# Kernel optimization log

Measured on AMD Instinct MI355X. Metric: run time of the kernel, lower is better.

The kernel has to match this reference:

```python
import jax, jax.numpy as jnp
import numpy as np

N_NODES = 20000
N_EDGES = 160000
N_GRAPHS = 64
HIDDEN = 128
CTX = 2048
HEADS = 4
NUM_LAYERS = 3
NUM_BINS = 240
MAX_DIST = 30.0
GAMMA = 0.5
BN_EPS = 1e-5
OUT_DIM = 1024


def setup_inputs() -> dict:
    key = jax.random.key(0)
    ks = jax.random.split(key, 32)
    inp = {}
    inp["atom_types"] = jax.random.randint(ks[0], (N_NODES,), 0, 118)
    inp["pos"] = jax.random.normal(ks[1], (N_NODES, 3), dtype=jnp.float32) * 5.0
    inp["edge_index"] = jax.random.randint(ks[2], (2, N_EDGES), 0, N_NODES)
    inp["edge_attr"] = jax.random.uniform(ks[3], (N_EDGES, 5), dtype=jnp.float32)
    inp["batch"] = jnp.sort(jax.random.randint(ks[4], (N_NODES,), 0, N_GRAPHS))
    inp["context_vector"] = jax.random.normal(ks[5], (N_GRAPHS, CTX), dtype=jnp.float32)
    # initial node embedding Linear(118 -> 128)
    inp["emb_W"] = jax.random.normal(ks[6], (118, HIDDEN), dtype=jnp.float32) * 0.05
    inp["emb_b"] = jnp.zeros((HIDDEN,), jnp.float32)
    # RBF positional MLP: Linear(720->128) + BN + ReLU + Linear(128->2048)
    inp["rbf_lin1_W"] = jax.random.normal(ks[7], (3 * NUM_BINS, 128), dtype=jnp.float32) * 0.03
    inp["rbf_lin1_b"] = jnp.zeros((128,), jnp.float32)
    inp["rbf_bn_g"] = jnp.ones((128,), jnp.float32)
    inp["rbf_bn_b"] = jnp.zeros((128,), jnp.float32)
    inp["rbf_bn_m"] = jax.random.normal(ks[8], (128,), dtype=jnp.float32) * 0.1
    inp["rbf_bn_v"] = jax.random.uniform(ks[9], (128,), dtype=jnp.float32, minval=0.5, maxval=1.5)
    inp["rbf_lin2_W"] = jax.random.normal(ks[10], (128, CTX), dtype=jnp.float32) * 0.05
    inp["rbf_lin2_b"] = jnp.zeros((CTX,), jnp.float32)
    # per-layer GAT params (stacked over layers)
    in_dim = HIDDEN + CTX  # 2176
    inp["gat_W"] = jax.random.normal(ks[11], (NUM_LAYERS, in_dim, HEADS * HIDDEN), dtype=jnp.float32) * 0.02
    inp["att_src"] = jax.random.normal(ks[12], (NUM_LAYERS, HEADS, HIDDEN), dtype=jnp.float32) * 0.1
    inp["att_dst"] = jax.random.normal(ks[13], (NUM_LAYERS, HEADS, HIDDEN), dtype=jnp.float32) * 0.1
    inp["gat_bias"] = jnp.zeros((NUM_LAYERS, HIDDEN), jnp.float32)
    inp["bn_g"] = jnp.ones((NUM_LAYERS, HIDDEN), jnp.float32)
    inp["bn_b"] = jnp.zeros((NUM_LAYERS, HIDDEN), jnp.float32)
    inp["bn_m"] = jax.random.normal(ks[14], (NUM_LAYERS, HIDDEN), dtype=jnp.float32) * 0.1
    inp["bn_v"] = jax.random.uniform(ks[15], (NUM_LAYERS, HIDDEN), dtype=jnp.float32, minval=0.5, maxval=1.5)
    # final Linear(128 -> 1024)
    inp["out_W"] = jax.random.normal(ks[16], (HIDDEN, OUT_DIM), dtype=jnp.float32) * 0.05
    inp["out_b"] = jnp.zeros((OUT_DIM,), jnp.float32)
    return inp


def _bn_eval(x, g, b, m, v):
    return (x - m) * jax.lax.rsqrt(v + BN_EPS) * g + b


def _forward(atom_types, pos, edge_index, edge_attr, batch, context_vector,
             emb_W, emb_b, rbf_lin1_W, rbf_lin1_b, rbf_bn_g, rbf_bn_b, rbf_bn_m,
             rbf_bn_v, rbf_lin2_W, rbf_lin2_b, gat_W, att_src, att_dst, gat_bias,
             bn_g, bn_b, bn_m, bn_v, out_W, out_b):
    N = atom_types.shape[0]
    # initial node embedding (one-hot @ W == row gather, but keep faithful math)
    x = jax.nn.one_hot(atom_types, 118, dtype=jnp.float32) @ emb_W + emb_b  # [N,128]
    # RBF positional encoding: [N,3,num_bins] -> [N,720]
    mu = jnp.linspace(-MAX_DIST, MAX_DIST, NUM_BINS, dtype=jnp.float32)
    rbf = jnp.exp(-GAMMA * (pos[..., None] - mu) ** 2).reshape(N, 3 * NUM_BINS)
    h = jax.nn.relu(_bn_eval(rbf @ rbf_lin1_W + rbf_lin1_b, rbf_bn_g, rbf_bn_b, rbf_bn_m, rbf_bn_v))
    pos_emb = h @ rbf_lin2_W + rbf_lin2_b  # [N,2048]
    context = context_vector[batch] + pos_emb  # pos_info == 'add'
    # GAT adds self-loops by default; edge_attr is ignored (edge_dim=None)
    loops = jnp.arange(N)
    src = jnp.concatenate([edge_index[0], loops])  # message source j
    dst = jnp.concatenate([edge_index[1], loops])  # message target i
    for l in range(NUM_LAYERS):
        xc = jnp.concatenate([x, context], axis=1)                  # [N,2176]
        xs = (xc @ gat_W[l]).reshape(N, HEADS, HIDDEN)              # [N,H,C]
        a_src = jnp.einsum('nhc,hc->nh', xs, att_src[l])            # [N,H]
        a_dst = jnp.einsum('nhc,hc->nh', xs, att_dst[l])
        alpha = jax.nn.leaky_relu(a_src[src] + a_dst[dst], 0.2)     # [E+N,H]
        amax = jax.ops.segment_max(alpha, dst, num_segments=N)
        alpha = jnp.exp(alpha - amax[dst])
        denom = jax.ops.segment_sum(alpha, dst, num_segments=N)
        alpha = alpha / jnp.maximum(denom[dst], 1e-16)
        msg = xs[src] * alpha[..., None]                             # [E+N,H,C]
        agg = jax.ops.segment_sum(msg, dst, num_segments=N)          # [N,H,C]
        x_conv = agg.mean(axis=1) + gat_bias[l]                      # concat=False -> head mean
        x_conv = _bn_eval(x_conv, bn_g[l], bn_b[l], bn_m[l], bn_v[l])
        x_conv = jax.nn.gelu(x_conv, approximate=False)
        x = x + x_conv                                               # residual; dropout inactive (eval)
    out = x @ out_W + out_b                                          # [N,1024]
    return jax.ops.segment_sum(out, batch, num_segments=N_GRAPHS)    # global_add_pool -> [B,1024]


def reference(atom_types, pos, edge_index, edge_attr, batch, context_vector,
              emb_W, emb_b, rbf_lin1_W, rbf_lin1_b, rbf_bn_g, rbf_bn_b, rbf_bn_m,
              rbf_bn_v, rbf_lin2_W, rbf_lin2_b, gat_W, att_src, att_dst, gat_bias,
              bn_g, bn_b, bn_m, bn_v, out_W, out_b):
    return _forward(atom_types, pos, edge_index, edge_attr, batch, context_vector,
                    emb_W, emb_b, rbf_lin1_W, rbf_lin1_b, rbf_bn_g, rbf_bn_b,
                    rbf_bn_m, rbf_bn_v, rbf_lin2_W, rbf_lin2_b, gat_W, att_src,
                    att_dst, gat_bias, bn_g, bn_b, bn_m, bn_v, out_W, out_b)
```

## Files before the change

### kernel.cpp

```cpp
#include <hip/hip_runtime.h>
#include <hip/hip_bf16.h>
#include <cstdint>

constexpr int HIDDEN = 128, CTXD = 2048, HEADS = 4, NLAYERS = 3;
constexpr int KRBF = 720, KPAD = 736;
constexpr int KXH = 256;

typedef __bf16 bf16x8 __attribute__((ext_vector_type(8)));
typedef float f32x4 __attribute__((ext_vector_type(4)));

static __device__ __forceinline__ unsigned short f2bf(float f) {
    union { float f; unsigned u; } v; v.f = f;
    unsigned r = v.u + 0x7fffu + ((v.u >> 16) & 1u);
    return (unsigned short)(r >> 16);
}
static __device__ __forceinline__ float bf2f(unsigned short s) {
    union { unsigned u; float f; } v; v.u = ((unsigned)s) << 16; return v.f;
}

__global__ __launch_bounds__(256) void k_tr(const float* __restrict__ src,
                                            unsigned short* __restrict__ dst,
                                            int R, int C) {
    __shared__ unsigned short t[32][34];
    int b = blockIdx.z;
    int c0 = blockIdx.x * 32, r0 = blockIdx.y * 32;
    const float* s = src + (size_t)b * R * C;
    unsigned short* d = dst + (size_t)b * R * C;
    for (int rr = threadIdx.y; rr < 32; rr += 8) {
        int r = r0 + rr, c = c0 + threadIdx.x;
        unsigned short val = 0;
        if (r < R && c < C) val = f2bf(s[(size_t)r * C + c]);
        t[rr][threadIdx.x] = val;
    }
    __syncthreads();
    for (int rr = threadIdx.y; rr < 32; rr += 8) {
        int c = c0 + rr, r = r0 + threadIdx.x;
        if (c < C && r < R) d[(size_t)c * R + r] = t[threadIdx.x][rr];
    }
}

__global__ __launch_bounds__(256) void k_w2bf(const float* __restrict__ W2,
                                              unsigned short* __restrict__ W2bf) {
    int i = blockIdx.x * 256 + threadIdx.x;
    if (i < 128 * CTXD) W2bf[i] = f2bf(W2[i]);
}
__global__ __launch_bounds__(256) void k_cpre(const float* __restrict__ ctx,
                                              const float* __restrict__ b2,
                                              unsigned short* __restrict__ cpre, int NG) {
    int i = blockIdx.x * 256 + threadIdx.x;
    if (i < NG * CTXD) cpre[i] = f2bf(ctx[i] + b2[i % CTXD]);
}
__global__ __launch_bounds__(256) void k_bccopy(const unsigned short* __restrict__ gatWt,
                                                unsigned short* __restrict__ Bc) {
    int i = blockIdx.x * 256 + threadIdx.x;
    if (i >= NLAYERS * 512 * 128) return;
    int lo = i >> 7, k = i & 127;
    Bc[(size_t)lo * KXH + k] = gatWt[(size_t)lo * 2176 + k];
}

__global__ __launch_bounds__(256) void k_trW1(const float* __restrict__ W1,
                                              unsigned short* __restrict__ W1t) {
    int i = blockIdx.x * 256 + threadIdx.x;
    if (i >= 128 * KPAD) return;
    int c = i / KPAD, k = i % KPAD;
    unsigned short v = 0;
    if (k < KRBF) v = f2bf(W1[(size_t)k * 128 + c]);
    W1t[i] = v;
}

__global__ __launch_bounds__(256) void k_embed(const int* __restrict__ at,
                                               const float* __restrict__ W,
                                               const float* __restrict__ b,
                                               float* __restrict__ x,
                                               unsigned short* __restrict__ xh, int N) {
    int i = blockIdx.x * 256 + threadIdx.x;
    if (i >= N * HIDDEN) return;
    int n = i >> 7, c = i & 127;
    float v = W[(size_t)at[n] * HIDDEN + c] + b[c];
    x[i] = v;
    xh[(size_t)n * KXH + c] = f2bf(v);
}

__global__ __launch_bounds__(256) void k_rbf_mfma(const float* __restrict__ pos,
                                                  const unsigned short* __restrict__ W1t,
                                                  const float* __restrict__ b1,
                                                  const float* __restrict__ g,
                                                  const float* __restrict__ bb,
                                                  const float* __restrict__ bm,
                                                  const float* __restrict__ bv,
                                                  unsigned short* __restrict__ xh, int N) {
    constexpr int LDT = 40;
    __shared__ unsigned short As[128 * LDT];
    __shared__ unsigned short Bs[128 * LDT];
    __shared__ float ps[128 * 3];
    const int tid = threadIdx.x;
    const int lane = tid & 63, wid = tid >> 6;
    const int nb = blockIdx.x * 128;
    for (int i = tid; i < 384; i += 256) {
        int n = nb + i / 3;
        ps[i] = (n < N) ? pos[(size_t)n * 3 + (i % 3)] : 1.0e9f;
    }
    __syncthreads();
    const int sr = tid >> 1, sk = (tid & 1) * 16;
    const int wr = (wid >> 1) * 64, wc = (wid & 1) * 64;
    const int fr = lane & 15, kg = lane >> 4;
    f32x4 acc[4][4];
#pragma unroll
    for (int i = 0; i < 4; i++)
#pragma unroll
        for (int j = 0; j < 4; j++)
#pragma unroll
            for (int r = 0; r < 4; r++) acc[i][j][r] = 0.f;
    const float p0 = ps[sr * 3], p1 = ps[sr * 3 + 1], p2 = ps[sr * 3 + 2];
    const unsigned short* bp = W1t + (size_t)sr * KPAD + sk;
    uint4 bv0 = *(const uint4*)bp, bv1 = *(const uint4*)(bp + 8);
    constexpr int NST = KPAD / 32;
    for (int ks = 0; ks < NST; ++ks) {
        unsigned short av[16];
#pragma unroll
        for (int j = 0; j < 16; j++) {
            int kglob = ks * 32 + sk + j;
            float v = 0.f;
            if (kglob < KRBF) {
                int d = kglob / 240, bin = kglob % 240;
                float mu = -30.f + (60.f / 239.f) * (float)bin;
                float p = (d == 0) ? p0 : ((d == 1) ? p1 : p2);
                float df = p - mu;
                v = __expf(-0.5f * df * df);
            }
            av[j] = f2bf(v);
        }
        __syncthreads();
        *(uint4*)&As[sr * LDT + sk] = *(const uint4*)&av[0];
        *(uint4*)&As[sr * LDT + sk + 8] = *(const uint4*)&av[8];
        *(uint4*)&Bs[sr * LDT + sk] = bv0;
        *(uint4*)&Bs[sr * LDT + sk + 8] = bv1;
        __syncthreads();
        if (ks + 1 < NST) {
            const unsigned short* bp2 = W1t + (size_t)sr * KPAD + (ks + 1) * 32 + sk;
            bv0 = *(const uint4*)bp2;
            bv1 = *(const uint4*)(bp2 + 8);
        }
        bf16x8 afr[4], bfr[4];
#pragma unroll
        for (int i = 0; i < 4; i++) {
            afr[i] = *reinterpret_cast<const bf16x8*>(&As[(wr + i * 16 + fr) * LDT + kg * 8]);
            bfr[i] = *reinterpret_cast<const bf16x8*>(&Bs[(wc + i * 16 + fr) * LDT + kg * 8]);
        }
#pragma unroll
        for (int i = 0; i < 4; i++)
#pragma unroll
            for (int j = 0; j < 4; j++)
                acc[i][j] = __builtin_amdgcn_mfma_f32_16x16x32_bf16(afr[i], bfr[j], acc[i][j], 0, 0, 0);
    }
    const int rg = lane >> 4;
#pragma unroll
    for (int i = 0; i < 4; i++) {
#pragma unroll
        for (int j = 0; j < 4; j++) {
            int col = wc + j * 16 + fr;
            float sc = g[col] * rsqrtf(bv[col] + 1e-5f);
            float sh = bb[col] - bm[col] * sc;
            float bc = b1[col];
#pragma unroll
            for (int r = 0; r < 4; r++) {
                int row = nb + wr + i * 16 + rg * 4 + r;
                if (row < N) {
                    float y = (acc[i][j][r] + bc) * sc + sh;
                    y = fmaxf(y, 0.f);
                    xh[(size_t)row * KXH + 128 + col] = f2bf(y);
                }
            }
        }
    }
}

template <int MODE, int DOATT>
__device__ __forceinline__ void gemm_core(unsigned short* As, unsigned short* Bs,
                                          const unsigned short* __restrict__ A, int lda, int M,
                                          const unsigned short* __restrict__ Bt, int ldb, int K,
                                          void* __restrict__ Cout, int ldc,
                                          const int* __restrict__ batch,
                                          const float* __restrict__ cw,
                                          int m0, int n0,
                                          const float* __restrict__ att_s,
                                          const float* __restrict__ att_d,
                                          float* __restrict__ a_src,
                                          float* __restrict__ a_dst) {
    constexpr int LDT = 40;
    const int tid = threadIdx.x;
    const int lane = tid & 63, wid = tid >> 6;
    const int wr = (wid >> 1) * 64, wc = (wid & 1) * 64;
    const int sr = tid >> 1, sk = (tid & 1) * 16;
    f32x4 acc[4][4];
#pragma unroll
    for (int i = 0; i < 4; i++)
#pragma unroll
        for (int j = 0; j < 4; j++)
#pragma unroll
            for (int r = 0; r < 4; r++) acc[i][j][r] = 0.f;
    const int nst = K / 32;
    const int arow = min(m0 + sr, M - 1);
    const unsigned short* ap = A + (size_t)arow * lda + sk;
    const unsigned short* bp = Bt + (size_t)(n0 + sr) * ldb + sk;
    uint4 av0 = *(const uint4*)ap, av1 = *(const uint4*)(ap + 8);
    uint4 bv0 = *(const uint4*)bp, bv1 = *(const uint4*)(bp + 8);
    const int fr = lane & 15, kg = lane >> 4;
    for (int ks = 0; ks < nst; ++ks) {
        __syncthreads();
        *(uint4*)&As[sr * LDT + sk] = av0;
        *(uint4*)&As[sr * LDT + sk + 8] = av1;
        *(uint4*)&Bs[sr * LDT + sk] = bv0;
        *(uint4*)&Bs[sr * LDT + sk + 8] = bv1;
        __syncthreads();
        if (ks + 1 < nst) {
            const unsigned short* ap2 = A + (size_t)arow * lda + (ks + 1) * 32 + sk;
            const unsigned short* bp2 = Bt + (size_t)(n0 + sr) * ldb + (ks + 1) * 32 + sk;
            av0 = *(const uint4*)ap2; av1 = *(const uint4*)(ap2 + 8);
            bv0 = *(const uint4*)bp2; bv1 = *(const uint4*)(bp2 + 8);
        }
        bf16x8 afr[4], bfr[4];
#pragma unroll
        for (int i = 0; i < 4; i++) {
            afr[i] = *reinterpret_cast<const bf16x8*>(&As[(wr + i * 16 + fr) * LDT + kg * 8]);
            bfr[i] = *reinterpret_cast<const bf16x8*>(&Bs[(wc + i * 16 + fr) * LDT + kg * 8]);
        }
#pragma unroll
        for (int i = 0; i < 4; i++)
#pragma unroll
            for (int j = 0; j < 4; j++)
                acc[i][j] = __builtin_amdgcn_mfma_f32_16x16x32_bf16(afr[i], bfr[j], acc[i][j], 0, 0, 0);
    }
    const int rg = lane >> 4;
    float pssum[4][4], pdsum[4][4];
#pragma unroll
    for (int i = 0; i < 4; i++)
#pragma unroll
        for (int r = 0; r < 4; r++) { pssum[i][r] = 0.f; pdsum[i][r] = 0.f; }
#pragma unroll
    for (int i = 0; i < 4; i++) {
#pragma unroll
        for (int j = 0; j < 4; j++) {
            int col = n0 + wc + j * 16 + fr;
            float asw = 0.f, adw = 0.f;
            if (DOATT) { asw = att_s[col]; adw = att_d[col]; }
#pragma unroll
            for (int r = 0; r < 4; r++) {
                int row = m0 + wr + i * 16 + rg * 4 + r;
                if (row < M) {
                    float vv = acc[i][j][r];
                    if (MODE == 2) {
                        ((float*)Cout)[(size_t)row * ldc + col] = vv;
                    } else if (MODE == 3) {
                        vv += cw[(size_t)batch[row] * 512 + col];
                        ((unsigned short*)Cout)[(size_t)row * ldc + col] = f2bf(vv);
                        if (DOATT) { pssum[i][r] += vv * asw; pdsum[i][r] += vv * adw; }
                    } else {
                        ((unsigned short*)Cout)[(size_t)row * ldc + col] = f2bf(vv);
                    }
                }
            }
        }
    }
    if (DOATT) {
        __syncthreads();
        float* lat = (float*)As;
#pragma unroll
        for (int i = 0; i < 4; i++) {
#pragma unroll
            for (int r = 0; r < 4; r++) {
                float s = pssum[i][r], d = pdsum[i][r];
#pragma unroll
                for (int dd = 1; dd < 16; dd <<= 1) {
                    s += __shfl_xor(s, dd);
                    d += __shfl_xor(d, dd);
                }
                if (fr == 0) {
                    int k = i * 16 + rg * 4 + r;
                    lat[(wid * 64 + k) * 2] = s;
                    lat[(wid * 64 + k) * 2 + 1] = d;
                }
            }
        }
        __syncthreads();
        if ((wid & 1) == 0) {
            int k = lane;
            int row = m0 + (wid >> 1) * 64 + k;
            if (row < M) {
                float s = lat[(wid * 64 + k) * 2] + lat[((wid + 1) * 64 + k) * 2];
                float d = lat[(wid * 64 + k) * 2 + 1] + lat[((wid + 1) * 64 + k) * 2 + 1];
                int head = n0 >> 7;
                a_src[(size_t)row * 4 + head] = s;
                a_dst[(size_t)row * 4 + head] = d;
            }
        }
    }
}

__global__ __launch_bounds__(256) void k_gemm3(const unsigned short* __restrict__ A, int M,
                                               const unsigned short* __restrict__ Bt,
                                               unsigned short* __restrict__ C,
                                               const int* __restrict__ batch,
                                               const float* __restrict__ cw,
                                               const float* __restrict__ att_s,
                                               const float* __restrict__ att_d,
                                               float* __restrict__ a_src,
                                               float* __restrict__ a_dst) {
    constexpr int LDT = 40;
    __shared__ unsigned short As[128 * LDT];
    __shared__ unsigned short Bs[128 * LDT];
    gemm_core<3, 1>(As, Bs, A, KXH, M, Bt, KXH, KXH, C, 512, batch, cw,
                    blockIdx.x * 128, blockIdx.y * 128, att_s, att_d, a_src, a_dst);
}

__global__ __launch_bounds__(256) void k_prep(const unsigned short* __restrict__ gatWt,
                                              const unsigned short* __restrict__ W2bf,
                                              const unsigned short* __restrict__ cpre,
                                              unsigned short* __restrict__ Bc,
                                              float* __restrict__ cW, int NG) {
    constexpr int LDT = 40;
    __shared__ unsigned short As[128 * LDT];
    __shared__ unsigned short Bs[128 * LDT];
    int z = blockIdx.z;
    if (z < 3) {
        if (blockIdx.y != 0) return;
        gemm_core<0, 0>(As, Bs, gatWt + (size_t)z * 512 * 2176 + 128, 2176, 512,
                        W2bf, CTXD, CTXD, Bc + (size_t)z * 512 * KXH + 128, KXH,
                        nullptr, nullptr, blockIdx.x * 128, 0,
                        nullptr, nullptr, nullptr, nullptr);
    } else {
        if (blockIdx.x != 0) return;
        int zz = z - 3;
        gemm_core<2, 0>(As, Bs, cpre, CTXD, NG, gatWt + (size_t)zz * 512 * 2176 + 128, 2176, CTXD,
                        cW + (size_t)zz * NG * 512, 512, nullptr, nullptr, 0, blockIdx.y * 128,
                        nullptr, nullptr, nullptr, nullptr);
    }
}

__global__ void k_cnt_init(int* cnt, int N) {
    int i = blockIdx.x * 256 + threadIdx.x;
    if (i < N) cnt[i] = 1;
}
__global__ void k_cnt(const int* __restrict__ ei, int E, int* cnt) {
    int i = blockIdx.x * 256 + threadIdx.x;
    if (i < E) atomicAdd(&cnt[ei[E + i]], 1);
}
__global__ __launch_bounds__(1024) void k_scan(const int* __restrict__ cnt, int* __restrict__ rowptr,
                                               int* __restrict__ cursor, int n) {
    __shared__ int wsum[16];
    __shared__ int carry;
    int tid = threadIdx.x, lane = tid & 63, wid = tid >> 6;
    if (tid == 0) carry = 0;
    __syncthreads();
    for (int basei = 0; basei < n; basei += 1024) {
        int i = basei + tid;
        int v = (i < n) ? cnt[i] : 0;
        int s = v;
#pragma unroll
        for (int d = 1; d < 64; d <<= 1) {
            int t = __shfl_up(s, (unsigned)d);
            if (lane >= d) s += t;
        }
        if (lane == 63) wsum[wid] = s;
        __syncthreads();
        if (wid == 0 && lane < 16) {
            int ws = wsum[lane]; int t = ws;
#pragma unroll
            for (int d = 1; d < 16; d <<= 1) {
                int u = __shfl_up(t, (unsigned)d);
                if (lane >= d) t += u;
            }
            wsum[lane] = t - ws;
        }
        __syncthreads();
        int excl = carry + wsum[wid] + (s - v);
        if (i < n) { rowptr[i] = excl; cursor[i] = excl; }
        __syncthreads();
        if (tid == 1023) carry += wsum[15] + s;
        __syncthreads();
    }
    if (tid == 0) rowptr[n] = carry;
}
__global__ void k_fill(const int* __restrict__ ei, int E, int N, int* cursor, int* csrc) {
    int i = blockIdx.x * 256 + threadIdx.x;
    if (i >= E + N) return;
    int s, d;
    if (i < E) { s = ei[i]; d = ei[E + i]; }
    else { s = i - E; d = s; }
    int slot = atomicAdd(&cursor[d], 1);
    csrc[slot] = s;
}

__global__ __launch_bounds__(256) void k_agg(const int* __restrict__ rowptr,
                                             const int* __restrict__ csrc,
                                             const float* __restrict__ asrc,
                                             const float* __restrict__ adstv,
                                             const unsigned short* __restrict__ xs,
                                             const float* __restrict__ gbias,
                                             const float* __restrict__ bg,
                                             const float* __restrict__ bb,
                                             const float* __restrict__ bm,
                                             const float* __restrict__ bv,
                                             float* __restrict__ x,
                                             unsigned short* __restrict__ xh, int N) {
    __shared__ float wsh[4][64][4];
    __shared__ int ssh[4][64];
    int tid = threadIdx.x, lane = tid & 63, wid = tid >> 6;
    int n = blockIdx.x * 4 + wid;
    if (n >= N) return;
    int beg = rowptr[n], end = rowptr[n + 1];
    float4 ad = *(const float4*)(adstv + (size_t)n * 4);
    int nch = (end - beg + 63) >> 6;
    float m0 = -1e30f, m1 = -1e30f, m2 = -1e30f, m3 = -1e30f;
    float s0 = 0.f, s1 = 0.f, s2 = 0.f, s3 = 0.f;
    float a0 = -1e30f, a1 = -1e30f, a2 = -1e30f, a3 = -1e30f;
    int sv = 0;
    for (int base = beg; base < end; base += 64) {
        int idx = base + lane;
        float b0 = -1e30f, b1 = -1e30f, b2 = -1e30f, b3 = -1e30f;
        int s = 0;
        if (idx < end) {
            s = csrc[idx];
            float4 t = *(const float4*)(asrc + (size_t)s * 4);
            b0 = t.x + ad.x; b0 = b0 > 0.f ? b0 : 0.2f * b0;
            b1 = t.y + ad.y; b1 = b1 > 0.f ? b1 : 0.2f * b1;
            b2 = t.z + ad.z; b2 = b2 > 0.f ? b2 : 0.2f * b2;
            b3 = t.w + ad.w; b3 = b3 > 0.f ? b3 : 0.2f * b3;
        }
        float c0 = b0, c1 = b1, c2 = b2, c3 = b3;
#pragma unroll
        for (int d = 1; d < 64; d <<= 1) {
            c0 = fmaxf(c0, __shfl_xor(c0, d));
            c1 = fmaxf(c1, __shfl_xor(c1, d));
            c2 = fmaxf(c2, __shfl_xor(c2, d));
            c3 = fmaxf(c3, __shfl_xor(c3, d));
        }
        float nm0 = fmaxf(m0, c0), nm1 = fmaxf(m1, c1), nm2 = fmaxf(m2, c2), nm3 = fmaxf(m3, c3);
        float e0 = (idx < end) ? __expf(b0 - nm0) : 0.f;
        float e1 = (idx < end) ? __expf(b1 - nm1) : 0.f;
        float e2 = (idx < end) ? __expf(b2 - nm2) : 0.f;
        float e3 = (idx < end) ? __expf(b3 - nm3) : 0.f;
#pragma unroll
        for (int d = 1; d < 64; d <<= 1) {
            e0 += __shfl_xor(e0, d); e1 += __shfl_xor(e1, d);
            e2 += __shfl_xor(e2, d); e3 += __shfl_xor(e3, d);
        }
        s0 = s0 * __expf(m0 - nm0) + e0; m0 = nm0;
        s1 = s1 * __expf(m1 - nm1) + e1; m1 = nm1;
        s2 = s2 * __expf(m2 - nm2) + e2; m2 = nm2;
        s3 = s3 * __expf(m3 - nm3) + e3; m3 = nm3;
        a0 = b0; a1 = b1; a2 = b2; a3 = b3; sv = s;
    }
    float i0 = 1.f / fmaxf(s0, 1e-16f), i1 = 1.f / fmaxf(s1, 1e-16f);
    float i2 = 1.f / fmaxf(s2, 1e-16f), i3 = 1.f / fmaxf(s3, 1e-16f);
    const int h = lane >> 4, c0i = (lane & 15) * 8;
    float acc[8];
#pragma unroll
    for (int j = 0; j < 8; j++) acc[j] = 0.f;
    for (int base = beg; base < end; base += 64) {
        int s; float w0, w1, w2, w3;
        if (nch == 1) {
            s = sv;
            w0 = __expf(a0 - m0) * i0; w1 = __expf(a1 - m1) * i1;
            w2 = __expf(a2 - m2) * i2; w3 = __expf(a3 - m3) * i3;
        } else {
            int idx = base + lane;
            float b0 = -1e30f, b1 = -1e30f, b2 = -1e30f, b3 = -1e30f;
            s = 0;
            if (idx < end) {
                s = csrc[idx];
                float4 t = *(const float4*)(asrc + (size_t)s * 4);
                b0 = t.x + ad.x; b0 = b0 > 0.f ? b0 : 0.2f * b0;
                b1 = t.y + ad.y; b1 = b1 > 0.f ? b1 : 0.2f * b1;
                b2 = t.z + ad.z; b2 = b2 > 0.f ? b2 : 0.2f * b2;
                b3 = t.w + ad.w; b3 = b3 > 0.f ? b3 : 0.2f * b3;
            }
            w0 = __expf(b0 - m0) * i0; w1 = __expf(b1 - m1) * i1;
            w2 = __expf(b2 - m2) * i2; w3 = __expf(b3 - m3) * i3;
        }
        ssh[wid][lane] = s;
        wsh[wid][lane][0] = w0; wsh[wid][lane][1] = w1;
        wsh[wid][lane][2] = w2; wsh[wid][lane][3] = w3;
        int cnt = min(64, end - base);
        int i = 0;
        for (; i + 2 <= cnt; i += 2) {
            int sa = ssh[wid][i], sb = ssh[wid][i + 1];
            float wa = wsh[wid][i][h], wb = wsh[wid][i + 1][h];
            uint4 ra = *(const uint4*)(xs + ((size_t)sa << 9) + (h << 7) + c0i);
            uint4 rb = *(const uint4*)(xs + ((size_t)sb << 9) + (h << 7) + c0i);
            const unsigned short* qa = (const unsigned short*)&ra;
            const unsigned short* qb = (const unsigned short*)&rb;
#pragma unroll
            for (int j = 0; j < 8; j++) acc[j] += wa * bf2f(qa[j]);
#pragma unroll
            for (int j = 0; j < 8; j++) acc[j] += wb * bf2f(qb[j]);
        }
        if (i < cnt) {
            int sa = ssh[wid][i];
            float wa = wsh[wid][i][h];
            uint4 ra = *(const uint4*)(xs + ((size_t)sa << 9) + (h << 7) + c0i);
            const unsigned short* qa = (const unsigned short*)&ra;
#pragma unroll
            for (int j = 0; j < 8; j++) acc[j] += wa * bf2f(qa[j]);
        }
    }
#pragma unroll
    for (int j = 0; j < 8; j++) {
        acc[j] += __shfl_xor(acc[j], 16);
        acc[j] += __shfl_xor(acc[j], 32);
    }
    if (lane < 16) {
#pragma unroll
        for (int j = 0; j < 8; j++) {
            int c = c0i + j;
            float t = acc[j] * 0.25f + gbias[c];
            float sc = bg[c] * rsqrtf(bv[c] + 1e-5f);
            float y = (t - bm[c]) * sc + bb[c];
            float ge = 0.5f * y * (1.f + erff(y * 0.70710678118f));
            float xn = x[(size_t)n * 128 + c] + ge;
            x[(size_t)n * 128 + c] = xn;
            xh[(size_t)n * KXH + c] = f2bf(xn);
        }
    }
}

__global__ __launch_bounds__(256) void k_pool(const float* __restrict__ x,
                                              const int* __restrict__ batch,
                                              const float* __restrict__ W,
                                              const float* __restrict__ bo,
                                              float* __restrict__ out, int N) {
    __shared__ float xg[128];
    __shared__ float tmp[256];
    __shared__ int bounds[2];
    int g = blockIdx.x, tid = threadIdx.x;
    if (tid < 2) {
        int key = g + tid, lo = 0, hi = N;
        while (lo < hi) { int mid = (lo + hi) >> 1; if (batch[mid] < key) lo = mid + 1; else hi = mid; }
        bounds[tid] = lo;
    }
    __syncthreads();
    int s = bounds[0], e = bounds[1];
    int c = tid & 127, rgp = tid >> 7;
    float a = 0.f;
    for (int n = s + rgp; n < e; n += 2) a += x[(size_t)n * 128 + c];
    tmp[tid] = a;
    __syncthreads();
    if (tid < 128) xg[tid] = tmp[tid] + tmp[tid + 128];
    __syncthreads();
    float cntf = (float)(e - s);
    for (int j = tid; j < 1024; j += 256) {
        float o = cntf * bo[j];
        for (int cc = 0; cc < 128; cc++) o += xg[cc] * W[(size_t)cc * 1024 + j];
        out[(size_t)g * 1024 + j] = o;
    }
}

extern "C" void kernel_launch(void* const* d_in, const int* in_sizes, int n_in,
                              void* d_out, int out_size, void* d_ws, size_t ws_size,
                              hipStream_t stream) {
    const int N = in_sizes[0];
    const int E = in_sizes[2] / 2;
    const int NG = in_sizes[5] / CTXD;
    const int* at = (const int*)d_in[0];
    const float* pos = (const float*)d_in[1];
    const int* ei = (const int*)d_in[2];
    const int* batch = (const int*)d_in[4];
    const float* ctx = (const float*)d_in[5];
    const float* embW = (const float*)d_in[6];
    const float* embB = (const float*)d_in[7];
    const float* W1 = (const float*)d_in[8];
    const float* b1 = (const float*)d_in[9];
    const float* rg = (const float*)d_in[10];
    const float* rb = (const float*)d_in[11];
    const float* rm = (const float*)d_in[12];
    const float* rv = (const float*)d_in[13];
    const float* W2 = (const float*)d_in[14];
    const float* b2 = (const float*)d_in[15];
    const float* gatW = (const float*)d_in[16];
    const float* atts = (const float*)d_in[17];
    const float* attd = (const float*)d_in[18];
    const float* gbias = (const float*)d_in[19];
    const float* bg = (const float*)d_in[20];
    const float* bbb = (const float*)d_in[21];
    const float* bm = (const float*)d_in[22];
    const float* bv = (const float*)d_in[23];
    const float* outW = (const float*)d_in[24];
    const float* outb = (const float*)d_in[25];
    float* out = (float*)d_out;

    char* basep = (char*)d_ws;
    size_t off = 0;
    auto alloc = [&](size_t bytes) -> char* {
        char* p = basep + off;
        off = (off + bytes + 255) & ~(size_t)255;
        return p;
    };
    unsigned short* xh = (unsigned short*)alloc((size_t)N * KXH * 2);
    float* x = (float*)alloc((size_t)N * 128 * 4);
    unsigned short* xs = (unsigned short*)alloc((size_t)N * 512 * 2);
    float* a_src = (float*)alloc((size_t)N * 4 * 4);
    float* a_dst = (float*)alloc((size_t)N * 4 * 4);
    int* cnt = (int*)alloc((size_t)N * 4);
    int* rowptr = (int*)alloc((size_t)(N + 1) * 4);
    int* cursor = (int*)alloc((size_t)N * 4);
    int* csrc = (int*)alloc((size_t)(E + N) * 4);
    unsigned short* gatWt = (unsigned short*)alloc((size_t)NLAYERS * 512 * 2176 * 2);
    unsigned short* W1t = (unsigned short*)alloc((size_t)128 * KPAD * 2);
    unsigned short* W2bf = (unsigned short*)alloc((size_t)128 * CTXD * 2);
    unsigned short* cpre = (unsigned short*)alloc((size_t)NG * CTXD * 2);
    unsigned short* Bc = (unsigned short*)alloc((size_t)NLAYERS * 512 * KXH * 2);
    float* cW = (float*)alloc((size_t)NLAYERS * NG * 512 * 4);
    (void)ws_size; (void)n_in; (void)out_size;

    {
        dim3 b(32, 8);
        dim3 g1((512 + 31) / 32, (2176 + 31) / 32, NLAYERS);
        k_tr<<<g1, b, 0, stream>>>(gatW, gatWt, 2176, 512);
        k_trW1<<<(128 * KPAD + 255) / 256, 256, 0, stream>>>(W1, W1t);
        k_w2bf<<<(128 * CTXD + 255) / 256, 256, 0, stream>>>(W2, W2bf);
        k_cpre<<<(NG * CTXD + 255) / 256, 256, 0, stream>>>(ctx, b2, cpre, NG);
        k_bccopy<<<(NLAYERS * 512 * 128 + 255) / 256, 256, 0, stream>>>(gatWt, Bc);
        dim3 gp(4, 4, 6);
        k_prep<<<gp, 256, 0, stream>>>(gatWt, W2bf, cpre, Bc, cW, NG);
    }
    k_embed<<<(N * 128 + 255) / 256, 256, 0, stream>>>(at, embW, embB, x, xh, N);
    k_rbf_mfma<<<(N + 127) / 128, 256, 0, stream>>>(pos, W1t, b1, rg, rb, rm, rv, xh, N);
    k_cnt_init<<<(N + 255) / 256, 256, 0, stream>>>(cnt, N);
    k_cnt<<<(E + 255) / 256, 256, 0, stream>>>(ei, E, cnt);
    k_scan<<<1, 1024, 0, stream>>>(cnt, rowptr, cursor, N);
    k_fill<<<(E + N + 255) / 256, 256, 0, stream>>>(ei, E, N, cursor, csrc);
    {
        dim3 g((N + 127) / 128, 4, 1);
        for (int l = 0; l < NLAYERS; l++) {
            k_gemm3<<<g, 256, 0, stream>>>(xh, N, Bc + (size_t)l * 512 * KXH,
                                           xs, batch, cW + (size_t)l * NG * 512,
                                           atts + l * 512, attd + l * 512, a_src, a_dst);
            k_agg<<<(N + 3) / 4, 256, 0, stream>>>(rowptr, csrc, a_src, a_dst, xs,
                                                   gbias + l * 128, bg + l * 128, bbb + l * 128,
                                                   bm + l * 128, bv + l * 128, x, xh, N);
        }
    }
    k_pool<<<NG, 256, 0, stream>>>(x, batch, outW, outb, out, N);
}
```

Measured before the change: 474.7 us.

## Merge preprocessing kernels into combined launches and unroll aggregation gathers by eight

Weight conversion, the transposes, context prep, count init and embedding now run as block ranges of one `k_misc` launch. The RBF MLP, the Bc copy and the prep GEMMs share a second launch, `k_rbfprep`. This cuts the number of small kernel launches and lets independent preprocessing run in parallel. In the GAT aggregation loop, neighbour gathers are unrolled by eight with clamped indices and zeroed weights for the tail. That issues more independent loads at once, at the cost of higher register pressure and some redundant loads on short neighbour lists.

```diff
diff --git a/kernel.cpp b/kernel.cpp
--- a/kernel.cpp
+++ b/kernel.cpp
@@ -18,159 +18,66 @@
     union { unsigned u; float f; } v; v.u = ((unsigned)s) << 16; return v.f;
 }
 
-__global__ __launch_bounds__(256) void k_tr(const float* __restrict__ src,
-                                            unsigned short* __restrict__ dst,
-                                            int R, int C) {
+__global__ __launch_bounds__(256) void k_misc(const float* __restrict__ W1,
+                                              unsigned short* __restrict__ W1t,
+                                              const float* __restrict__ W2,
+                                              unsigned short* __restrict__ W2bf,
+                                              const float* __restrict__ ctx,
+                                              const float* __restrict__ b2,
+                                              unsigned short* __restrict__ cpre,
+                                              int* __restrict__ cnt,
+                                              const int* __restrict__ at,
+                                              const float* __restrict__ embW,
+                                              const float* __restrict__ embB,
+                                              float* __restrict__ x,
+                                              unsigned short* __restrict__ xh,
+                                              const float* __restrict__ gatW,
+                                              unsigned short* __restrict__ gatWt,
+                                              int N, int NG,
+                                              int e0, int e1, int e2, int e3, int e4) {
     __shared__ unsigned short t[32][34];
-    int b = blockIdx.z;
-    int c0 = blockIdx.x * 32, r0 = blockIdx.y * 32;
-    const float* s = src + (size_t)b * R * C;
-    unsigned short* d = dst + (size_t)b * R * C;
-    for (int rr = threadIdx.y; rr < 32; rr += 8) {
-        int r = r0 + rr, c = c0 + threadIdx.x;
-        unsigned short val = 0;
-        if (r < R && c < C) val = f2bf(s[(size_t)r * C + c]);
-        t[rr][threadIdx.x] = val;
-    }
-    __syncthreads();
-    for (int rr = threadIdx.y; rr < 32; rr += 8) {
-        int c = c0 + rr, r = r0 + threadIdx.x;
-        if (c < C && r < R) d[(size_t)c * R + r] = t[threadIdx.x][rr];
-    }
-}
-
-__global__ __launch_bounds__(256) void k_w2bf(const float* __restrict__ W2,
-                                              unsigned short* __restrict__ W2bf) {
-    int i = blockIdx.x * 256 + threadIdx.x;
-    if (i < 128 * CTXD) W2bf[i] = f2bf(W2[i]);
-}
-__global__ __launch_bounds__(256) void k_cpre(const float* __restrict__ ctx,
-                                              const float* __restrict__ b2,
-                                              unsigned short* __restrict__ cpre, int NG) {
-    int i = blockIdx.x * 256 + threadIdx.x;
-    if (i < NG * CTXD) cpre[i] = f2bf(ctx[i] + b2[i % CTXD]);
-}
-__global__ __launch_bounds__(256) void k_bccopy(const unsigned short* __restrict__ gatWt,
-                                                unsigned short* __restrict__ Bc) {
-    int i = blockIdx.x * 256 + threadIdx.x;
-    if (i >= NLAYERS * 512 * 128) return;
-    int lo = i >> 7, k = i & 127;
-    Bc[(size_t)lo * KXH + k] = gatWt[(size_t)lo * 2176 + k];
-}
-
-__global__ __launch_bounds__(256) void k_trW1(const float* __restrict__ W1,
-                                              unsigned short* __restrict__ W1t) {
-    int i = blockIdx.x * 256 + threadIdx.x;
-    if (i >= 128 * KPAD) return;
-    int c = i / KPAD, k = i % KPAD;
-    unsigned short v = 0;
-    if (k < KRBF) v = f2bf(W1[(size_t)k * 128 + c]);
-    W1t[i] = v;
-}
-
-__global__ __launch_bounds__(256) void k_embed(const int* __restrict__ at,
-                                               const float* __restrict__ W,
-                                               const float* __restrict__ b,
-                                               float* __restrict__ x,
-                                               unsigned short* __restrict__ xh, int N) {
-    int i = blockIdx.x * 256 + threadIdx.x;
-    if (i >= N * HIDDEN) return;
-    int n = i >> 7, c = i & 127;
-    float v = W[(size_t)at[n] * HIDDEN + c] + b[c];
-    x[i] = v;
-    xh[(size_t)n * KXH + c] = f2bf(v);
-}
-
-__global__ __launch_bounds__(256) void k_rbf_mfma(const float* __restrict__ pos,
-                                                  const unsigned short* __restrict__ W1t,
-                                                  const float* __restrict__ b1,
-                                                  const float* __restrict__ g,
-                                                  const float* __restrict__ bb,
-                                                  const float* __restrict__ bm,
-                                                  const float* __restrict__ bv,
-                                                  unsigned short* __restrict__ xh, int N) {
-    constexpr int LDT = 40;
-    __shared__ unsigned short As[128 * LDT];
-    __shared__ unsigned short Bs[128 * LDT];
-    __shared__ float ps[128 * 3];
-    const int tid = threadIdx.x;
-    const int lane = tid & 63, wid = tid >> 6;
-    const int nb = blockIdx.x * 128;
-    for (int i = tid; i < 384; i += 256) {
-        int n = nb + i / 3;
-        ps[i] = (n < N) ? pos[(size_t)n * 3 + (i % 3)] : 1.0e9f;
-    }
-    __syncthreads();
-    const int sr = tid >> 1, sk = (tid & 1) * 16;
-    const int wr = (wid >> 1) * 64, wc = (wid & 1) * 64;
-    const int fr = lane & 15, kg = lane >> 4;
-    f32x4 acc[4][4];
-#pragma unroll
-    for (int i = 0; i < 4; i++)
-#pragma unroll
-        for (int j = 0; j < 4; j++)
-#pragma unroll
-            for (int r = 0; r < 4; r++) acc[i][j][r] = 0.f;
-    const float p0 = ps[sr * 3], p1 = ps[sr * 3 + 1], p2 = ps[sr * 3 + 2];
-    const unsigned short* bp = W1t + (size_t)sr * KPAD + sk;
-    uint4 bv0 = *(const uint4*)bp, bv1 = *(const uint4*)(bp + 8);
-    constexpr int NST = KPAD / 32;
-    for (int ks = 0; ks < NST; ++ks) {
-        unsigned short av[16];
-#pragma unroll
-        for (int j = 0; j < 16; j++) {
-            int kglob = ks * 32 + sk + j;
-            float v = 0.f;
-            if (kglob < KRBF) {
-                int d = kglob / 240, bin = kglob % 240;
-                float mu = -30.f + (60.f / 239.f) * (float)bin;
-                float p = (d == 0) ? p0 : ((d == 1) ? p1 : p2);
-                float df = p - mu;
-                v = __expf(-0.5f * df * df);
-            }
-            av[j] = f2bf(v);
-        }
-        __syncthreads();
-        *(uint4*)&As[sr * LDT + sk] = *(const uint4*)&av[0];
-        *(uint4*)&As[sr * LDT + sk + 8] = *(const uint4*)&av[8];
-        *(uint4*)&Bs[sr * LDT + sk] = bv0;
-        *(uint4*)&Bs[sr * LDT + sk + 8] = bv1;
-        __syncthreads();
-        if (ks + 1 < NST) {
-            const unsigned short* bp2 = W1t + (size_t)sr * KPAD + (ks + 1) * 32 + sk;
-            bv0 = *(const uint4*)bp2;
-            bv1 = *(const uint4*)(bp2 + 8);
-        }
-        bf16x8 afr[4], bfr[4];
-#pragma unroll
-        for (int i = 0; i < 4; i++) {
-            afr[i] = *reinterpret_cast<const bf16x8*>(&As[(wr + i * 16 + fr) * LDT + kg * 8]);
-            bfr[i] = *reinterpret_cast<const bf16x8*>(&Bs[(wc + i * 16 + fr) * LDT + kg * 8]);
-        }
-#pragma unroll
-        for (int i = 0; i < 4; i++)
-#pragma unroll
-            for (int j = 0; j < 4; j++)
-                acc[i][j] = __builtin_amdgcn_mfma_f32_16x16x32_bf16(afr[i], bfr[j], acc[i][j], 0, 0, 0);
-    }
-    const int rg = lane >> 4;
-#pragma unroll
-    for (int i = 0; i < 4; i++) {
-#pragma unroll
-        for (int j = 0; j < 4; j++) {
-            int col = wc + j * 16 + fr;
-            float sc = g[col] * rsqrtf(bv[col] + 1e-5f);
-            float sh = bb[col] - bm[col] * sc;
-            float bc = b1[col];
-#pragma unroll
-            for (int r = 0; r < 4; r++) {
-                int row = nb + wr + i * 16 + rg * 4 + r;
-                if (row < N) {
-                    float y = (acc[i][j][r] + bc) * sc + sh;
-                    y = fmaxf(y, 0.f);
-                    xh[(size_t)row * KXH + 128 + col] = f2bf(y);
-                }
-            }
+    int b = blockIdx.x, tid = threadIdx.x;
+    if (b < e0) {
+        int i = b * 256 + tid;
+        if (i < 128 * KPAD) {
+            int c = i / KPAD, k = i % KPAD;
+            W1t[i] = (k < KRBF) ? f2bf(W1[(size_t)k * 128 + c]) : (unsigned short)0;
+        }
+    } else if (b < e1) {
+        int i = (b - e0) * 256 + tid;
+        if (i < 128 * CTXD) W2bf[i] = f2bf(W2[i]);
+    } else if (b < e2) {
+        int i = (b - e1) * 256 + tid;
+        if (i < NG * CTXD) cpre[i] = f2bf(ctx[i] + b2[i % CTXD]);
+    } else if (b < e3) {
+        int i = (b - e2) * 256 + tid;
+        if (i < N) cnt[i] = 1;
+    } else if (b < e4) {
+        int i = (b - e3) * 256 + tid;
+        if (i < N * HIDDEN) {
+            int n = i >> 7, c = i & 127;
+            float v = embW[(size_t)at[n] * HIDDEN + c] + embB[c];
+            x[i] = v;
+            xh[(size_t)n * KXH + c] = f2bf(v);
+        }
+    } else {
+        int idx = b - e4;
+        int bz = idx / (16 * 68);
+        int rem = idx % (16 * 68);
+        int bx = rem % 16, by = rem / 16;
+        int tx = tid & 31, ty = tid >> 5;
+        const int R = 2176, C = 512;
+        int c0 = bx * 32, r0 = by * 32;
+        const float* s = gatW + (size_t)bz * R * C;
+        unsigned short* d = gatWt + (size_t)bz * R * C;
+        for (int rr = ty; rr < 32; rr += 8) {
+            int r = r0 + rr, c = c0 + tx;
+            t[rr][tx] = f2bf(s[(size_t)r * C + c]);
+        }
+        __syncthreads();
+        for (int rr = ty; rr < 32; rr += 8) {
+            int c = c0 + rr, r = r0 + tx;
+            d[(size_t)c * R + r] = t[tx][rr];
         }
     }
 }
@@ -297,6 +204,128 @@
     }
 }
 
+__global__ __launch_bounds__(256) void k_rbfprep(const float* __restrict__ pos,
+                                                 const unsigned short* __restrict__ W1t,
+                                                 const float* __restrict__ b1,
+                                                 const float* __restrict__ g,
+                                                 const float* __restrict__ bb,
+                                                 const float* __restrict__ bm,
+                                                 const float* __restrict__ bv,
+                                                 unsigned short* __restrict__ xh,
+                                                 const unsigned short* __restrict__ gatWt,
+                                                 const unsigned short* __restrict__ W2bf,
+                                                 const unsigned short* __restrict__ cpre,
+                                                 unsigned short* __restrict__ Bc,
+                                                 float* __restrict__ cW,
+                                                 int N, int NG, int nbRbf) {
+    constexpr int LDT = 40;
+    __shared__ unsigned short As[128 * LDT];
+    __shared__ unsigned short Bs[128 * LDT];
+    __shared__ float ps[128 * 3];
+    const int bid = blockIdx.x;
+    const int tid = threadIdx.x;
+    if (bid >= nbRbf) {
+        int idx = bid - nbRbf;
+        if (idx < 12) {
+            int z = idx >> 2, mt = idx & 3;
+            gemm_core<0, 0>(As, Bs, gatWt + (size_t)z * 512 * 2176 + 128, 2176, 512,
+                            W2bf, CTXD, CTXD, Bc + (size_t)z * 512 * KXH + 128, KXH,
+                            nullptr, nullptr, mt * 128, 0, nullptr, nullptr, nullptr, nullptr);
+        } else if (idx < 24) {
+            int z = (idx - 12) >> 2, nt = (idx - 12) & 3;
+            gemm_core<2, 0>(As, Bs, cpre, CTXD, NG, gatWt + (size_t)z * 512 * 2176 + 128, 2176,
+                            CTXD, cW + (size_t)z * NG * 512, 512, nullptr, nullptr, 0, nt * 128,
+                            nullptr, nullptr, nullptr, nullptr);
+        } else {
+            int i = (idx - 24) * 256 + tid;
+            if (i < NLAYERS * 512 * 128) {
+                int lo = i >> 7, k = i & 127;
+                Bc[(size_t)lo * KXH + k] = gatWt[(size_t)lo * 2176 + k];
+            }
+        }
+        return;
+    }
+    const int lane = tid & 63, wid = tid >> 6;
+    const int nb = bid * 128;
+    for (int i = tid; i < 384; i += 256) {
+        int n = nb + i / 3;
+        ps[i] = (n < N) ? pos[(size_t)n * 3 + (i % 3)] : 1.0e9f;
+    }
+    __syncthreads();
+    const int sr = tid >> 1, sk = (tid & 1) * 16;
+    const int wr = (wid >> 1) * 64, wc = (wid & 1) * 64;
+    const int fr = lane & 15, kg = lane >> 4;
+    f32x4 acc[4][4];
+#pragma unroll
+    for (int i = 0; i < 4; i++)
+#pragma unroll
+        for (int j = 0; j < 4; j++)
+#pragma unroll
+            for (int r = 0; r < 4; r++) acc[i][j][r] = 0.f;
+    const float p0 = ps[sr * 3], p1 = ps[sr * 3 + 1], p2 = ps[sr * 3 + 2];
+    const unsigned short* bp = W1t + (size_t)sr * KPAD + sk;
+    uint4 bv0 = *(const uint4*)bp, bv1 = *(const uint4*)(bp + 8);
+    constexpr int NST = KPAD / 32;
+    for (int ks = 0; ks < NST; ++ks) {
+        unsigned short av[16];
+#pragma unroll
+        for (int j = 0; j < 16; j++) {
+            int kglob = ks * 32 + sk + j;
+            float v = 0.f;
+            if (kglob < KRBF) {
+                int d = kglob / 240, bin = kglob % 240;
+                float mu = -30.f + (60.f / 239.f) * (float)bin;
+                float p = (d == 0) ? p0 : ((d == 1) ? p1 : p2);
+                float df = p - mu;
+                v = __expf(-0.5f * df * df);
+            }
+            av[j] = f2bf(v);
+        }
+        __syncthreads();
+        *(uint4*)&As[sr * LDT + sk] = *(const uint4*)&av[0];
+        *(uint4*)&As[sr * LDT + sk + 8] = *(const uint4*)&av[8];
+        *(uint4*)&Bs[sr * LDT + sk] = bv0;
+        *(uint4*)&Bs[sr * LDT + sk + 8] = bv1;
+        __syncthreads();
+        if (ks + 1 < NST) {
+            const unsigned short* bp2 = W1t + (size_t)sr * KPAD + (ks + 1) * 32 + sk;
+            bv0 = *(const uint4*)bp2;
+            bv1 = *(const uint4*)(bp2 + 8);
+        }
+        bf16x8 afr[4], bfr[4];
+#pragma unroll
+        for (int i = 0; i < 4; i++) {
+            afr[i] = *reinterpret_cast<const bf16x8*>(&As[(wr + i * 16 + fr) * LDT + kg * 8]);
+            bfr[i] = *reinterpret_cast<const bf16x8*>(&Bs[(wc + i * 16 + fr) * LDT + kg * 8]);
+        }
+#pragma unroll
+        for (int i = 0; i < 4; i++)
+#pragma unroll
+            for (int j = 0; j < 4; j++)
+                acc[i][j] = __builtin_amdgcn_mfma_f32_16x16x32_bf16(afr[i], bfr[j], acc[i][j], 0, 0, 0);
+    }
+    const int rg = lane >> 4;
+#pragma unroll
+    for (int i = 0; i < 4; i++) {
+#pragma unroll
+        for (int j = 0; j < 4; j++) {
+            int col = wc + j * 16 + fr;
+            float sc = g[col] * rsqrtf(bv[col] + 1e-5f);
+            float sh = bb[col] - bm[col] * sc;
+            float bc = b1[col];
+#pragma unroll
+            for (int r = 0; r < 4; r++) {
+                int row = nb + wr + i * 16 + rg * 4 + r;
+                if (row < N) {
+                    float y = (acc[i][j][r] + bc) * sc + sh;
+                    y = fmaxf(y, 0.f);
+                    xh[(size_t)row * KXH + 128 + col] = f2bf(y);
+                }
+            }
+        }
+    }
+}
+
 __global__ __launch_bounds__(256) void k_gemm3(const unsigned short* __restrict__ A, int M,
                                                const unsigned short* __restrict__ Bt,
                                                unsigned short* __restrict__ C,
@@ -313,34 +342,6 @@
                     blockIdx.x * 128, blockIdx.y * 128, att_s, att_d, a_src, a_dst);
 }
 
-__global__ __launch_bounds__(256) void k_prep(const unsigned short* __restrict__ gatWt,
-                                              const unsigned short* __restrict__ W2bf,
-                                              const unsigned short* __restrict__ cpre,
-                                              unsigned short* __restrict__ Bc,
-                                              float* __restrict__ cW, int NG) {
-    constexpr int LDT = 40;
-    __shared__ unsigned short As[128 * LDT];
-    __shared__ unsigned short Bs[128 * LDT];
-    int z = blockIdx.z;
-    if (z < 3) {
-        if (blockIdx.y != 0) return;
-        gemm_core<0, 0>(As, Bs, gatWt + (size_t)z * 512 * 2176 + 128, 2176, 512,
-                        W2bf, CTXD, CTXD, Bc + (size_t)z * 512 * KXH + 128, KXH,
-                        nullptr, nullptr, blockIdx.x * 128, 0,
-                        nullptr, nullptr, nullptr, nullptr);
-    } else {
-        if (blockIdx.x != 0) return;
-        int zz = z - 3;
-        gemm_core<2, 0>(As, Bs, cpre, CTXD, NG, gatWt + (size_t)zz * 512 * 2176 + 128, 2176, CTXD,
-                        cW + (size_t)zz * NG * 512, 512, nullptr, nullptr, 0, blockIdx.y * 128,
-                        nullptr, nullptr, nullptr, nullptr);
-    }
-}
-
-__global__ void k_cnt_init(int* cnt, int N) {
-    int i = blockIdx.x * 256 + threadIdx.x;
-    if (i < N) cnt[i] = 1;
-}
 __global__ void k_cnt(const int* __restrict__ ei, int E, int* cnt) {
     int i = blockIdx.x * 256 + threadIdx.x;
     if (i < E) atomicAdd(&cnt[ei[E + i]], 1);
@@ -482,26 +483,24 @@
         wsh[wid][lane][0] = w0; wsh[wid][lane][1] = w1;
         wsh[wid][lane][2] = w2; wsh[wid][lane][3] = w3;
         int cnt = min(64, end - base);
-        int i = 0;
-        for (; i + 2 <= cnt; i += 2) {
-            int sa = ssh[wid][i], sb = ssh[wid][i + 1];
-            float wa = wsh[wid][i][h], wb = wsh[wid][i + 1][h];
-            uint4 ra = *(const uint4*)(xs + ((size_t)sa << 9) + (h << 7) + c0i);
-            uint4 rb = *(const uint4*)(xs + ((size_t)sb << 9) + (h << 7) + c0i);
-            const unsigned short* qa = (const unsigned short*)&ra;
-            const unsigned short* qb = (const unsigned short*)&rb;
-#pragma unroll
-            for (int j = 0; j < 8; j++) acc[j] += wa * bf2f(qa[j]);
-#pragma unroll
-            for (int j = 0; j < 8; j++) acc[j] += wb * bf2f(qb[j]);
-        }
-        if (i < cnt) {
-            int sa = ssh[wid][i];
-            float wa = wsh[wid][i][h];
-            uint4 ra = *(const uint4*)(xs + ((size_t)sa << 9) + (h << 7) + c0i);
-            const unsigned short* qa = (const unsigned short*)&ra;
-#pragma unroll
-            for (int j = 0; j < 8; j++) acc[j] += wa * bf2f(qa[j]);
+        for (int i = 0; i < cnt; i += 8) {
+            int sa[8]; float wa[8];
+#pragma unroll
+            for (int u = 0; u < 8; u++) {
+                int ii = min(i + u, cnt - 1);
+                sa[u] = ssh[wid][ii];
+                wa[u] = (i + u < cnt) ? wsh[wid][ii][h] : 0.f;
+            }
+            uint4 ra[8];
+#pragma unroll
+            for (int u = 0; u < 8; u++)
+                ra[u] = *(const uint4*)(xs + ((size_t)sa[u] << 9) + (h << 7) + c0i);
+#pragma unroll
+            for (int u = 0; u < 8; u++) {
+                const unsigned short* q = (const unsigned short*)&ra[u];
+#pragma unroll
+                for (int j = 0; j < 8; j++) acc[j] += wa[u] * bf2f(q[j]);
+            }
         }
     }
 #pragma unroll
@@ -613,20 +612,25 @@
     (void)ws_size; (void)n_in; (void)out_size;
 
     {
-        dim3 b(32, 8);
-        dim3 g1((512 + 31) / 32, (2176 + 31) / 32, NLAYERS);
-        k_tr<<<g1, b, 0, stream>>>(gatW, gatWt, 2176, 512);
-        k_trW1<<<(128 * KPAD + 255) / 256, 256, 0, stream>>>(W1, W1t);
-        k_w2bf<<<(128 * CTXD + 255) / 256, 256, 0, stream>>>(W2, W2bf);
-        k_cpre<<<(NG * CTXD + 255) / 256, 256, 0, stream>>>(ctx, b2, cpre, NG);
-        k_bccopy<<<(NLAYERS * 512 * 128 + 255) / 256, 256, 0, stream>>>(gatWt, Bc);
-        dim3 gp(4, 4, 6);
-        k_prep<<<gp, 256, 0, stream>>>(gatWt, W2bf, cpre, Bc, cW, NG);
-    }
-    k_embed<<<(N * 128 + 255) / 256, 256, 0, stream>>>(at, embW, embB, x, xh, N);
-    k_rbf_mfma<<<(N + 127) / 128, 256, 0, stream>>>(pos, W1t, b1, rg, rb, rm, rv, xh, N);
-    k_cnt_init<<<(N + 255) / 256, 256, 0, stream>>>(cnt, N);
+        int nbW1t = (128 * KPAD + 255) / 256;
+        int nbW2 = (128 * CTXD + 255) / 256;
+        int nbCp = (NG * CTXD + 255) / 256;
+        int nbCi = (N + 255) / 256;
+        int nbEm = (N * 128 + 255) / 256;
+        int nbTr = 16 * 68 * 3;
+        int e0 = nbW1t, e1 = e0 + nbW2, e2 = e1 + nbCp, e3 = e2 + nbCi, e4 = e3 + nbEm;
+        int total = e4 + nbTr;
+        k_misc<<<total, 256, 0, stream>>>(W1, W1t, W2, W2bf, ctx, b2, cpre, cnt,
+                                          at, embW, embB, x, xh, gatW, gatWt,
+                                          N, NG, e0, e1, e2, e3, e4);
+    }
     k_cnt<<<(E + 255) / 256, 256, 0, stream>>>(ei, E, cnt);
+    {
+        int nbRbf = (N + 127) / 128;
+        int nbBc = (NLAYERS * 512 * 128 + 255) / 256;
+        k_rbfprep<<<nbRbf + 24 + nbBc, 256, 0, stream>>>(pos, W1t, b1, rg, rb, rm, rv, xh,
+                                                         gatWt, W2bf, cpre, Bc, cW, N, NG, nbRbf);
+    }
     k_scan<<<1, 1024, 0, stream>>>(cnt, rowptr, cursor, N);
     k_fill<<<(E + N + 255) / 256, 256, 0, stream>>>(ei, E, N, cursor, csrc);
     {
```

After: 456.7 us. 3.8% less time.
